# Optimization experiments

Hardware: AMD Instinct MI355X
Metric: run time of the kernel (lower is better)

Reference implementation:

```python
import jax, jax.numpy as jnp
import numpy as np

WIN = (16, 9, 9)
WIN_SIZE = WIN[0] * WIN[1] * WIN[2]  # 1296
EPS = float(np.e ** -15)             # ~3.06e-7, matches np.power(np.e, -15)


def setup_inputs() -> dict:
    key = jax.random.key(0)
    k1, k2 = jax.random.split(key)
    shape = (2, 1, 96, 192, 192)  # [B, 1, D, H, W]
    I = jax.random.normal(k1, shape, dtype=jnp.float32)
    J = jax.random.normal(k2, shape, dtype=jnp.float32)
    return {"I": I, "J": J}


def _box_sums(tmp):
    # Grouped conv3d with an all-ones [5,1,16,9,9] kernel: per-channel sliding
    k = jnp.ones((5, 1) + WIN, dtype=tmp.dtype)
    return jax.lax.conv_general_dilated(
        tmp, k,
        window_strides=(1, 1, 1),
        padding=[(0, 0), (WIN[1] // 2, WIN[1] // 2), (WIN[2] // 2, WIN[2] // 2)],
        feature_group_count=5,
        dimension_numbers=("NCDHW", "OIDHW", "NCDHW"),
    )


def reference(I, J):
    # I, J: [B, 1, D, H, W]
    tmp = jnp.concatenate([I, J, I * I, J * J, I * J], axis=1)  # [B,5,D,H,W]
    sums = _box_sums(tmp)  # [B, 5, D-15, H, W]
    I_sum, J_sum = sums[:, 0], sums[:, 1]
    I2_sum, J2_sum, IJ_sum = sums[:, 2], sums[:, 3], sums[:, 4]

    u_I = I_sum / WIN_SIZE
    u_J = J_sum / WIN_SIZE

    cross = IJ_sum - u_J * I_sum - u_I * J_sum + u_I * u_J * WIN_SIZE
    I_var = I2_sum - 2.0 * u_I * I_sum + u_I * u_I * WIN_SIZE
    J_var = J2_sum - 2.0 * u_J * J_sum + u_J * u_J * WIN_SIZE

    nz = (I_var * J_var) > EPS  # bool_non_zero; where false, substitute 1.0
    cross = jnp.where(nz, cross, 1.0)
    I_var = jnp.where(nz, I_var, 1.0)
    J_var = jnp.where(nz, J_var, 1.0)

    cc = cross * cross / (I_var * J_var + EPS)  # [B, D-15, H, W]
    loss = -1.0 * jnp.mean(cc, axis=(1, 2, 3)) + 1.0  # [B]
    return loss, cc
```

## Files before the change

### kernel.cpp

```cpp
#include <hip/hip_runtime.h>


constexpr int N = 2, D = 96, H = 192, W = 192;
constexpr int OD = 81;
constexpr int KD = 16;
constexpr int HWp = H * W;
constexpr float INV_WIN = 1.0f / 1296.0f;
constexpr float EPS_NZ = 3.0590232050182579e-07f;
constexpr int CH = 24;
constexpr int ODPB = 14;

typedef __fp16 h2 __attribute__((ext_vector_type(2)));

__device__ __forceinline__ unsigned pkrtz(float lo, float hi) {
  h2 h = __builtin_amdgcn_cvt_pkrtz(lo, hi);
  unsigned u; __builtin_memcpy(&u, &h, 4); return u;
}
__device__ __forceinline__ h2 as_h2(unsigned u) {
  h2 h; __builtin_memcpy(&h, &u, 4); return h;
}
__device__ __forceinline__ unsigned as_u(h2 h) {
  unsigned u; __builtin_memcpy(&u, &h, 4); return u;
}
__device__ __forceinline__ unsigned bperm(int bidx, unsigned v) {
  return (unsigned)__builtin_amdgcn_ds_bpermute(bidx, (int)v);
}

__global__ __launch_bounds__(256)
void k_dw(const float* __restrict__ I, const float* __restrict__ J,
          unsigned* __restrict__ ws, int od0, int c, int odcStride) {
  const int h = blockIdx.x;
  const int n = blockIdx.z;
  const int os = od0 + blockIdx.y * ODPB;
  int oe = od0 + c; if (os + ODPB < oe) oe = os + ODPB;
  if (os >= oe) return;

  const int lane = threadIdx.x & 63;
  const int seg  = threadIdx.x >> 6;
  const int wcol = seg * 56 + lane - 4;
  const bool colOK = (wcol >= 0) && (wcol < W);
  const bool stOK  = (lane >= 4) && (lane < 60) && (wcol < W);

  const size_t colBase = ((size_t)n * D * H + h) * (size_t)W + wcol;
  const float* Ip = I + colBase;
  const float* Jp = J + colBase;
  unsigned* wbase = ws + ((size_t)n * odcStride * HWp + (size_t)h * W + wcol) * 3;

  const int im1 = ((lane - 1) & 63) << 2;
  const int ip1 = ((lane + 1) & 63) << 2;
  const int im3 = ((lane - 3) & 63) << 2;
  const int ip3 = ((lane + 3) & 63) << 2;

  float sI = 0.f, sJ = 0.f, sII = 0.f, sJJ = 0.f, sIJ = 0.f;
  for (int d = os; d < os + KD - 1; ++d) {
    const float iv = colOK ? Ip[(size_t)d * HWp] : 0.f;
    const float jv = colOK ? Jp[(size_t)d * HWp] : 0.f;
    sI += iv; sJ += jv;
    sII += iv * iv; sJJ += jv * jv; sIJ += iv * jv;
  }

  float eI = colOK ? Ip[(size_t)(os + KD - 1) * HWp] : 0.f;
  float eJ = colOK ? Jp[(size_t)(os + KD - 1) * HWp] : 0.f;
  float lI = colOK ? Ip[(size_t)os * HWp] : 0.f;
  float lJ = colOK ? Jp[(size_t)os * HWp] : 0.f;

  for (int od = os; od < oe; ++od) {
    const float ceI = eI, ceJ = eJ, clI = lI, clJ = lJ;
    const int odn = od + 1;
    if (odn < oe) {
      eI = colOK ? Ip[(size_t)(odn + KD - 1) * HWp] : 0.f;
      eJ = colOK ? Jp[(size_t)(odn + KD - 1) * HWp] : 0.f;
      lI = colOK ? Ip[(size_t)odn * HWp] : 0.f;
      lJ = colOK ? Jp[(size_t)odn * HWp] : 0.f;
    }
    sI += ceI; sJ += ceJ;
    sII += ceI * ceI; sJJ += ceJ * ceJ; sIJ += ceI * ceJ;
    const unsigned x0 = pkrtz(sI, sJ);
    const unsigned x1 = pkrtz(sII, sJJ);
    const unsigned x2 = pkrtz(sIJ, 0.f);
    sI -= clI; sJ -= clJ;
    sII -= clI * clI; sJJ -= clJ * clJ; sIJ -= clI * clJ;

    const unsigned a0 = as_u(as_h2(bperm(im1, x0)) + as_h2(x0) + as_h2(bperm(ip1, x0)));
    const unsigned a1 = as_u(as_h2(bperm(im1, x1)) + as_h2(x1) + as_h2(bperm(ip1, x1)));
    const unsigned a2 = as_u(as_h2(bperm(im1, x2)) + as_h2(x2) + as_h2(bperm(ip1, x2)));
    const unsigned r0 = as_u(as_h2(bperm(im3, a0)) + as_h2(a0) + as_h2(bperm(ip3, a0)));
    const unsigned r1 = as_u(as_h2(bperm(im3, a1)) + as_h2(a1) + as_h2(bperm(ip3, a1)));
    const unsigned r2 = as_u(as_h2(bperm(im3, a2)) + as_h2(a2) + as_h2(bperm(ip3, a2)));

    if (stOK) {
      unsigned* o = wbase + (size_t)(od - od0) * HWp * 3;
      o[0] = r0; o[1] = r1; o[2] = r2;
    }
  }
}

__global__ __launch_bounds__(192)
void k_hcc(const unsigned* __restrict__ ws, float* __restrict__ cc,
           float* __restrict__ acc, int od0, int odcStride) {
  const int odi = blockIdx.x;
  const int od = od0 + odi;
  const int h0 = blockIdx.y * CH;
  const int n = blockIdx.z;
  const int w = threadIdx.x;
  const unsigned* base =
      ws + ((size_t)n * odcStride * HWp + (size_t)odi * HWp + w) * 3;
  float* ccp = cc + ((size_t)n * OD + od) * (size_t)HWp + w;

  float s0 = 0.f, s1 = 0.f, s2 = 0.f, s3 = 0.f, s4 = 0.f;
  float lsum = 0.f;
  uint3 hist[8];
  const uint3 z3 = make_uint3(0u, 0u, 0u);

  uint3 vN = z3;
  {
    const int hin = h0 - 4;
    if (hin >= 0) vN = *(const uint3*)(base + (size_t)hin * W * 3);
  }
#pragma unroll
  for (int t = 0; t < CH + 8; ++t) {
    const uint3 v = vN;
    if (t + 1 < CH + 8) {
      const int hn = h0 - 4 + t + 1;
      vN = (hn >= 0 && hn < H) ? *(const uint3*)(base + (size_t)hn * W * 3) : z3;
    }
    {
      h2 v0 = as_h2(v.x), v1 = as_h2(v.y), v2 = as_h2(v.z);
      s0 += (float)v0[0]; s1 += (float)v0[1];
      s2 += (float)v1[0]; s3 += (float)v1[1];
      s4 += (float)v2[0];
    }
    if (t >= 8) {
      const int h = h0 + t - 8;
      const float cross = s4 - s0 * s1 * INV_WIN;
      const float vI = s2 - s0 * s0 * INV_WIN;
      const float vJ = s3 - s1 * s1 * INV_WIN;
      const float prod = vI * vJ;
      const float c = (prod > EPS_NZ) ? (cross * cross) / (prod + EPS_NZ)
                                      : 1.0f / (1.0f + EPS_NZ);
      ccp[(size_t)h * W] = c;
      lsum += c;
      const uint3 q = hist[t & 7];
      h2 q0 = as_h2(q.x), q1 = as_h2(q.y), q2 = as_h2(q.z);
      s0 -= (float)q0[0]; s1 -= (float)q0[1];
      s2 -= (float)q1[0]; s3 -= (float)q1[1];
      s4 -= (float)q2[0];
    }
    hist[t & 7] = v;
  }
  __shared__ float red[3];
#pragma unroll
  for (int off = 32; off > 0; off >>= 1) lsum += __shfl_xor(lsum, off, 64);
  if ((threadIdx.x & 63) == 0) red[threadIdx.x >> 6] = lsum;
  __syncthreads();
  if (threadIdx.x == 0) atomicAdd(acc + n, red[0] + red[1] + red[2]);
}

__global__ void k_fin(const float* __restrict__ acc, float* __restrict__ out) {
  if (threadIdx.x < N)
    out[threadIdx.x] = 1.0f - acc[threadIdx.x] * (1.0f / 2985984.0f);
}

extern "C" void kernel_launch(void* const* d_in, const int* in_sizes, int n_in,
                              void* d_out, int out_size, void* d_ws,
                              size_t ws_size, hipStream_t stream) {
  const float* I = (const float*)d_in[0];
  const float* J = (const float*)d_in[1];
  float* out = (float*)d_out;
  float* acc = (float*)d_ws;
  unsigned* planes = (unsigned*)((char*)d_ws + 256);

  hipMemsetAsync(d_ws, 0, 2 * sizeof(float), stream);

  const size_t perOdPerN = (size_t)HWp * 12;
  size_t avail = (ws_size > 256) ? (ws_size - 256) : 0;
  long long odcMax = (long long)(avail / (2 * perOdPerN));
  if (odcMax < 1) odcMax = 1;
  if (odcMax > OD) odcMax = OD;
  const int odc = (int)odcMax;

  float* ccOut = out + 2;
  for (int od0 = 0; od0 < OD; od0 += odc) {
    const int c = (odc < OD - od0) ? odc : (OD - od0);
    const int S = (c + ODPB - 1) / ODPB;
    hipLaunchKernelGGL(k_dw, dim3(H, S, N), dim3(256), 0, stream,
                       I, J, planes, od0, c, odc);
    hipLaunchKernelGGL(k_hcc, dim3(c, H / CH, N), dim3(192), 0, stream,
                       planes, ccOut, acc, od0, odc);
  }
  hipLaunchKernelGGL(k_fin, dim3(1), dim3(64), 0, stream, acc, out);
}
```

Measured before the change: 76.73 us.

## Switch intermediate box sums to fp32 LDS shuffles with bf16 storage

New measurement: 80.40 us. +4.8%, slower.

```diff
diff --git a/kernel.cpp b/kernel.cpp
--- a/kernel.cpp
+++ b/kernel.cpp
@@ -10,46 +10,39 @@
 constexpr int CH = 24;
 constexpr int ODPB = 14;
 
-typedef __fp16 h2 __attribute__((ext_vector_type(2)));
-
-__device__ __forceinline__ unsigned pkrtz(float lo, float hi) {
-  h2 h = __builtin_amdgcn_cvt_pkrtz(lo, hi);
-  unsigned u; __builtin_memcpy(&u, &h, 4); return u;
+__device__ __forceinline__ unsigned bf16rne(float f) {
+  unsigned u = __float_as_uint(f);
+  return (u + 0x7fffu + ((u >> 16) & 1u)) >> 16;
 }
-__device__ __forceinline__ h2 as_h2(unsigned u) {
-  h2 h; __builtin_memcpy(&h, &u, 4); return h;
-}
-__device__ __forceinline__ unsigned as_u(h2 h) {
-  unsigned u; __builtin_memcpy(&u, &h, 4); return u;
-}
-__device__ __forceinline__ unsigned bperm(int bidx, unsigned v) {
-  return (unsigned)__builtin_amdgcn_ds_bpermute(bidx, (int)v);
+__device__ __forceinline__ float bf16tof(unsigned h) {
+  return __uint_as_float(h << 16);
 }
 
-__global__ __launch_bounds__(256)
+__global__ __launch_bounds__(64)
 void k_dw(const float* __restrict__ I, const float* __restrict__ J,
           unsigned* __restrict__ ws, int od0, int c, int odcStride) {
-  const int h = blockIdx.x;
+  const int h = blockIdx.x >> 2;
+  const int tile = blockIdx.x & 3;
   const int n = blockIdx.z;
   const int os = od0 + blockIdx.y * ODPB;
   int oe = od0 + c; if (os + ODPB < oe) oe = os + ODPB;
   if (os >= oe) return;
 
-  const int lane = threadIdx.x & 63;
-  const int seg  = threadIdx.x >> 6;
-  const int wcol = seg * 56 + lane - 4;
+  const int lane = threadIdx.x;
+  const int wcol = tile * 56 + lane - 4;
   const bool colOK = (wcol >= 0) && (wcol < W);
   const bool stOK  = (lane >= 4) && (lane < 60) && (wcol < W);
+
+  __shared__ float4 x4[64]; __shared__ float x1[64];
+  __shared__ float4 a4[64]; __shared__ float a1[64];
 
   const size_t colBase = ((size_t)n * D * H + h) * (size_t)W + wcol;
   const float* Ip = I + colBase;
   const float* Jp = J + colBase;
   unsigned* wbase = ws + ((size_t)n * odcStride * HWp + (size_t)h * W + wcol) * 3;
 
-  const int im1 = ((lane - 1) & 63) << 2;
-  const int ip1 = ((lane + 1) & 63) << 2;
-  const int im3 = ((lane - 3) & 63) << 2;
-  const int ip3 = ((lane + 3) & 63) << 2;
+  const int lm1 = (lane - 1) & 63, lp1 = (lane + 1) & 63;
+  const int lm3 = (lane - 3) & 63, lp3 = (lane + 3) & 63;
 
   float sI = 0.f, sJ = 0.f, sII = 0.f, sJJ = 0.f, sIJ = 0.f;
   for (int d = os; d < os + KD - 1; ++d) {
@@ -75,22 +68,33 @@
     }
     sI += ceI; sJ += ceJ;
     sII += ceI * ceI; sJJ += ceJ * ceJ; sIJ += ceI * ceJ;
-    const unsigned x0 = pkrtz(sI, sJ);
-    const unsigned x1 = pkrtz(sII, sJJ);
-    const unsigned x2 = pkrtz(sIJ, 0.f);
+    const float cI = sI, cJ = sJ, cII = sII, cJJ = sJJ, cIJ = sIJ;
+    x4[lane] = make_float4(cI, cJ, cII, cJJ); x1[lane] = cIJ;
     sI -= clI; sJ -= clJ;
     sII -= clI * clI; sJJ -= clJ * clJ; sIJ -= clI * clJ;
 
-    const unsigned a0 = as_u(as_h2(bperm(im1, x0)) + as_h2(x0) + as_h2(bperm(ip1, x0)));
-    const unsigned a1 = as_u(as_h2(bperm(im1, x1)) + as_h2(x1) + as_h2(bperm(ip1, x1)));
-    const unsigned a2 = as_u(as_h2(bperm(im1, x2)) + as_h2(x2) + as_h2(bperm(ip1, x2)));
-    const unsigned r0 = as_u(as_h2(bperm(im3, a0)) + as_h2(a0) + as_h2(bperm(ip3, a0)));
-    const unsigned r1 = as_u(as_h2(bperm(im3, a1)) + as_h2(a1) + as_h2(bperm(ip3, a1)));
-    const unsigned r2 = as_u(as_h2(bperm(im3, a2)) + as_h2(a2) + as_h2(bperm(ip3, a2)));
+    const float4 m0 = x4[lm1], m2 = x4[lp1];
+    const float  p0 = x1[lm1], p2 = x1[lp1];
+    const float aI  = m0.x + cI  + m2.x;
+    const float aJ  = m0.y + cJ  + m2.y;
+    const float aII = m0.z + cII + m2.z;
+    const float aJJ = m0.w + cJJ + m2.w;
+    const float aIJ = p0   + cIJ + p2;
+    a4[lane] = make_float4(aI, aJ, aII, aJJ); a1[lane] = aIJ;
+
+    const float4 b0 = a4[lm3], b2 = a4[lp3];
+    const float  q0 = a1[lm3], q2 = a1[lp3];
+    const float r0 = b0.x + aI  + b2.x;
+    const float r1 = b0.y + aJ  + b2.y;
+    const float r2 = b0.z + aII + b2.z;
+    const float r3 = b0.w + aJJ + b2.w;
+    const float r4 = q0   + aIJ + q2;
 
     if (stOK) {
       unsigned* o = wbase + (size_t)(od - od0) * HWp * 3;
-      o[0] = r0; o[1] = r1; o[2] = r2;
+      o[0] = bf16rne(r0) | (bf16rne(r1) << 16);
+      o[1] = bf16rne(r2) | (bf16rne(r3) << 16);
+      o[2] = bf16rne(r4);
     }
   }
 }
@@ -124,12 +128,9 @@
       const int hn = h0 - 4 + t + 1;
       vN = (hn >= 0 && hn < H) ? *(const uint3*)(base + (size_t)hn * W * 3) : z3;
     }
-    {
-      h2 v0 = as_h2(v.x), v1 = as_h2(v.y), v2 = as_h2(v.z);
-      s0 += (float)v0[0]; s1 += (float)v0[1];
-      s2 += (float)v1[0]; s3 += (float)v1[1];
-      s4 += (float)v2[0];
-    }
+    s0 += bf16tof(v.x & 0xffffu); s1 += bf16tof(v.x >> 16);
+    s2 += bf16tof(v.y & 0xffffu); s3 += bf16tof(v.y >> 16);
+    s4 += bf16tof(v.z & 0xffffu);
     if (t >= 8) {
       const int h = h0 + t - 8;
       const float cross = s4 - s0 * s1 * INV_WIN;
@@ -141,10 +142,9 @@
       ccp[(size_t)h * W] = c;
       lsum += c;
       const uint3 q = hist[t & 7];
-      h2 q0 = as_h2(q.x), q1 = as_h2(q.y), q2 = as_h2(q.z);
-      s0 -= (float)q0[0]; s1 -= (float)q0[1];
-      s2 -= (float)q1[0]; s3 -= (float)q1[1];
-      s4 -= (float)q2[0];
+      s0 -= bf16tof(q.x & 0xffffu); s1 -= bf16tof(q.x >> 16);
+      s2 -= bf16tof(q.y & 0xffffu); s3 -= bf16tof(q.y >> 16);
+      s4 -= bf16tof(q.z & 0xffffu);
     }
     hist[t & 7] = v;
   }
@@ -153,12 +153,17 @@
   for (int off = 32; off > 0; off >>= 1) lsum += __shfl_xor(lsum, off, 64);
   if ((threadIdx.x & 63) == 0) red[threadIdx.x >> 6] = lsum;
   __syncthreads();
-  if (threadIdx.x == 0) atomicAdd(acc + n, red[0] + red[1] + red[2]);
+  if (threadIdx.x == 0)
+    atomicAdd(acc + n * 32 + (odi & 31), red[0] + red[1] + red[2]);
 }
 
 __global__ void k_fin(const float* __restrict__ acc, float* __restrict__ out) {
-  if (threadIdx.x < N)
-    out[threadIdx.x] = 1.0f - acc[threadIdx.x] * (1.0f / 2985984.0f);
+  const int t = threadIdx.x;
+  float v = acc[t];
+#pragma unroll
+  for (int off = 16; off > 0; off >>= 1) v += __shfl_xor(v, off, 32);
+  if (t == 0)  out[0] = 1.0f - v * (1.0f / 2985984.0f);
+  if (t == 32) out[1] = 1.0f - v * (1.0f / 2985984.0f);
 }
 
 extern "C" void kernel_launch(void* const* d_in, const int* in_sizes, int n_in,
@@ -170,7 +175,7 @@
   float* acc = (float*)d_ws;
   unsigned* planes = (unsigned*)((char*)d_ws + 256);
 
-  hipMemsetAsync(d_ws, 0, 2 * sizeof(float), stream);
+  hipMemsetAsync(d_ws, 0, 64 * sizeof(float), stream);
 
   const size_t perOdPerN = (size_t)HWp * 12;
   size_t avail = (ws_size > 256) ? (ws_size - 256) : 0;
@@ -183,7 +188,7 @@
   for (int od0 = 0; od0 < OD; od0 += odc) {
     const int c = (odc < OD - od0) ? odc : (OD - od0);
     const int S = (c + ODPB - 1) / ODPB;
-    hipLaunchKernelGGL(k_dw, dim3(H, S, N), dim3(256), 0, stream,
+    hipLaunchKernelGGL(k_dw, dim3(H * 4, S, N), dim3(64), 0, stream,
                        I, J, planes, od0, c, odc);
     hipLaunchKernelGGL(k_hcc, dim3(c, H / CH, N), dim3(192), 0, stream,
                        planes, ccOut, acc, od0, odc);
```
